# Performance work log

Hardware: AMD Instinct MI355X
Metric: run time of the kernel (lower is better)

Reference implementation:

```python
import jax, jax.numpy as jnp
import numpy as np
import itertools


def _dwconv(x, w, b, pad, dil):
    # depthwise conv3d, x: [B,C,H,W,D], w: [C,1,k,k,k]
    out = jax.lax.conv_general_dilated(
        x, w, (1, 1, 1), [(pad, pad)] * 3, rhs_dilation=(dil, dil, dil),
        dimension_numbers=('NCDHW', 'OIDHW', 'NCDHW'), feature_group_count=x.shape[1])
    return out + b[None, :, None, None, None]


def _conv(x, w, b, pad):
    out = jax.lax.conv_general_dilated(
        x, w, (1, 1, 1), [(pad, pad)] * 3,
        dimension_numbers=('NCDHW', 'OIDHW', 'NCDHW'))
    return out + b[None, :, None, None, None]


def _pw(x, w, b):
    # 1x1x1 conv: x [B,C,H,W,D], w [O,C]
    return jnp.einsum('bchwd,oc->bohwd', x, w) + b[None, :, None, None, None]


def _deform_conv3d(x, off_w, off_b, w, b):
    # DeformConvPack-style: offsets from a regular 3x3x3 conv, then
    # trilinearly-interpolated gather at (base + kernel tap + offset), then GEMM.
    B, C, H, W, D = x.shape
    K = 27
    dt = x.dtype
    off = _conv(x, off_w, off_b, 1).reshape(B, K, 3, H, W, D)  # per-tap (dh,dw,dd)
    gh = jnp.arange(H, dtype=dt)
    gw = jnp.arange(W, dtype=dt)
    gd = jnp.arange(D, dtype=dt)
    base = jnp.stack(jnp.meshgrid(gh, gw, gd, indexing='ij'), 0)  # [3,H,W,D]
    t = jnp.arange(-1, 2, dtype=dt)  # kernel taps, padding=1
    taps = jnp.stack(jnp.meshgrid(t, t, t, indexing='ij'), -1).reshape(K, 3)
    pos = base[None] + taps[:, :, None, None, None]  # [K,3,H,W,D]
    pos = pos[None] + off  # [B,K,3,H,W,D]
    i0 = jnp.floor(pos)
    frac = pos - i0  # [B,K,3,H,W,D]
    i0 = i0.astype(jnp.int32)
    N = H * W * D
    xf = x.reshape(B, C, N)
    hi = jnp.array([H - 1, W - 1, D - 1], jnp.int32)[None, None, :, None, None, None]
    acc = jnp.zeros((B, C, K * N), dt)
    for corner in itertools.product((0, 1), repeat=3):
        c = jnp.array(corner, jnp.int32)[None, None, :, None, None, None]
        idx = i0 + c
        wgt = jnp.prod(jnp.where(c == 1, frac, 1.0 - frac), axis=2)  # [B,K,H,W,D]
        valid = jnp.all((idx >= 0) & (idx <= hi), axis=2)
        ic = jnp.clip(idx, 0, hi)
        flat = (ic[:, :, 0] * W + ic[:, :, 1]) * D + ic[:, :, 2]  # [B,K,H,W,D]
        g = jnp.take_along_axis(xf, flat.reshape(B, 1, K * N), axis=2)  # [B,C,K*N]
        acc = acc + g * (wgt * valid.astype(dt)).reshape(B, 1, K * N)
    sampled = acc.reshape(B, C, K, N)
    out = jnp.einsum('bckn,ock->bon', sampled, w.reshape(w.shape[0], C, K))
    out = out + b[None, :, None]
    return out.reshape(B, -1, H, W, D)


def _forward(x, proj1_w, proj1_b, conv0_w, conv0_b, convsp_w, convsp_b,
             off_w, off_b, dcn_w, dcn_b, conv1_w, conv1_b, proj2_w, proj2_b,
             B, C, H, W, D):
    xv = jnp.transpose(x, (0, 2, 1)).reshape(B, C, H, W, D)
    shortcut = xv
    h = jax.nn.gelu(_pw(xv, proj1_w, proj1_b), approximate=False)
    u = h
    a = _dwconv(h, conv0_w, conv0_b, 2, 1)        # 5x5x5 depthwise
    a = _dwconv(a, convsp_w, convsp_b, 9, 3)      # 7x7x7 depthwise, dilation 3
    a = _deform_conv3d(a, off_w, off_b, dcn_w, dcn_b)
    a = _pw(a, conv1_w, conv1_b)
    h = u * a
    h = _pw(h, proj2_w, proj2_b)
    out = h + shortcut
    return jnp.transpose(out.reshape(B, C, H * W * D), (0, 2, 1))


def setup_inputs() -> dict:
    key = jax.random.key(0)
    ks = jax.random.split(key, 8)
    B, C, H, W, D = 1, 64, 32, 32, 32
    N = H * W * D
    r = lambda k, s, sc: jax.random.normal(k, s, jnp.float32) * np.float32(sc)
    inv = lambda f: 1.0 / np.sqrt(f)
    return {
        'x': jax.random.normal(ks[0], (B, N, C), jnp.float32),
        'proj1_w': r(ks[1], (C, C), inv(C)), 'proj1_b': jnp.zeros((C,), jnp.float32),
        'conv0_w': r(ks[2], (C, 1, 5, 5, 5), inv(125)), 'conv0_b': jnp.zeros((C,), jnp.float32),
        'convsp_w': r(ks[3], (C, 1, 7, 7, 7), inv(343)), 'convsp_b': jnp.zeros((C,), jnp.float32),
        'off_w': r(ks[4], (81, C, 3, 3, 3), 0.01 * inv(27 * C)), 'off_b': jnp.zeros((81,), jnp.float32),
        'dcn_w': r(ks[5], (C, C, 3, 3, 3), inv(27 * C)), 'dcn_b': jnp.zeros((C,), jnp.float32),
        'conv1_w': r(ks[6], (C, C), inv(C)), 'conv1_b': jnp.zeros((C,), jnp.float32),
        'proj2_w': r(ks[7], (C, C), inv(C)), 'proj2_b': jnp.zeros((C,), jnp.float32),
        'B': B, 'C': C, 'H': H, 'W': W, 'D': D,
    }


def reference(x, proj1_w, proj1_b, conv0_w, conv0_b, convsp_w, convsp_b,
              off_w, off_b, dcn_w, dcn_b, conv1_w, conv1_b, proj2_w, proj2_b,
              B, C, H, W, D):
    return _forward(x, proj1_w, proj1_b, conv0_w, conv0_b, convsp_w, convsp_b,
                    off_w, off_b, dcn_w, dcn_b, conv1_w, conv1_b, proj2_w, proj2_b,
                    B, C, H, W, D)
```

## Files before the change

### kernel.cpp

```cpp
#include <hip/hip_runtime.h>
#include <math.h>

#define NSP 32768
#define NCH 64

typedef _Float16 half8 __attribute__((ext_vector_type(8)));
typedef _Float16 half4 __attribute__((ext_vector_type(4)));
typedef _Float16 half2v __attribute__((ext_vector_type(2)));
typedef float f32x4 __attribute__((ext_vector_type(4)));

__global__ __launch_bounds__(256) void k_proj1m(const float* __restrict__ x,
        const half8* __restrict__ Wp1, const float* __restrict__ b,
        float* __restrict__ U) {
    __shared__ __align__(16) _Float16 Sx[64 * 72];
    int t = threadIdx.x;
    int n0 = blockIdx.x * 64;
    int lane = t & 63, wv = t >> 6;
    for (int i = wv; i < 64; i += 4) {
        float v = x[(size_t)(n0 + i) * 64 + lane];
        Sx[i * 72 + lane] = (_Float16)v;
    }
    __syncthreads();
    int pl = lane & 15, g = lane >> 4;
    int ob = wv;
    const half8* wbase = Wp1 + ob * 64 + lane;
    #pragma unroll
    for (int nt = 0; nt < 4; ++nt) {
        f32x4 acc4 = {0.f, 0.f, 0.f, 0.f};
        const _Float16* sb = &Sx[(nt * 16 + pl) * 72 + g * 8];
        #pragma unroll
        for (int kb = 0; kb < 2; ++kb) {
            half8 af = wbase[kb * 256];
            half8 bf = *(const half8*)(sb + kb * 32);
            acc4 = __builtin_amdgcn_mfma_f32_16x16x32_f16(af, bf, acc4, 0, 0, 0);
        }
        int n = n0 + nt * 16 + pl;
        #pragma unroll
        for (int r = 0; r < 4; ++r) {
            int o = ob * 16 + g * 4 + r;
            float a = acc4[r] + b[o];
            float gv = 0.5f * a * (1.0f + erff(a * 0.70710678118654752f));
            U[(size_t)o * NSP + n] = gv;
        }
    }
}

__global__ __launch_bounds__(256) void k_dw5(const float* __restrict__ in,
        const float* __restrict__ w, const float* __restrict__ b,
        float* __restrict__ out) {
    __shared__ float Sb5[2][20 * 38];
    int t = threadIdx.x;
    int bid = blockIdx.x;
    int blk = (bid & 7) * 128 + (bid >> 3);
    int c  = blk >> 4;
    int hq = (blk >> 1) & 7;
    int wq = blk & 1;
    int d  = t & 31;
    int wbloc = t >> 5;
    int wb = wq * 8 + wbloc;
    const float* wc = w + c * 125;
    const float* src = in + (size_t)c * NSP;

    for (int idx = t; idx < 160; idx += 256) {
        int bi = idx / 80, r = idx % 80;
        int wi = r >> 2, e = r & 3;
        int Dp = (e < 2) ? e : 32 + e;
        Sb5[bi][wi * 38 + Dp] = 0.f;
    }

    float bc = b[c];
    float acc[4][2];
    #pragma unroll
    for (int a = 0; a < 4; ++a) { acc[a][0] = bc; acc[a][1] = bc; }

    #define STAGE5(m)                                                        \
        { int hh_ = 4 * hq + (m) - 2;                                        \
          if ((unsigned)hh_ < 32u) {                                         \
            const float* row_ = src + (hh_ << 10);                           \
            for (int idx = t; idx < 160; idx += 256) {                       \
                int wi = idx >> 3, q = idx & 7;                              \
                int wj = 16 * wq - 2 + wi;                                   \
                float4 vv = make_float4(0.f, 0.f, 0.f, 0.f);                 \
                if ((unsigned)wj < 32u)                                      \
                    vv = *(const float4*)&row_[(wj << 5) + q * 4];           \
                float* dst = &Sb5[(m) & 1][wi * 38 + 2 + q * 4];             \
                dst[0] = vv.x; dst[1] = vv.y; dst[2] = vv.z; dst[3] = vv.w;  \
            } } }

    STAGE5(0)
    __syncthreads();
    #pragma unroll 1
    for (int m = 0; m < 8; ++m) {
        if (m < 7) STAGE5(m + 1)
        int hh = 4 * hq + m - 2;
        if ((unsigned)hh < 32u) {
            float v[6][5];
            const float* sb = &Sb5[m & 1][0];
            #pragma unroll
            for (int jc = 0; jc < 6; ++jc)
                #pragma unroll
                for (int l = 0; l < 5; ++l)
                    v[jc][l] = sb[(2 * wbloc + jc) * 38 + d + l];
            #pragma unroll
            for (int a = 0; a < 4; ++a) {
                if (a <= m && m <= a + 4) {
                    const float* wr = wc + (m - a) * 25;
                    float s0 = 0.f, s1 = 0.f;
                    #pragma unroll
                    for (int j = 0; j < 5; ++j)
                        #pragma unroll
                        for (int l = 0; l < 5; ++l) {
                            float wv2 = wr[j * 5 + l];
                            s0 += wv2 * v[j][l];
                            s1 += wv2 * v[j + 1][l];
                        }
                    acc[a][0] += s0;
                    acc[a][1] += s1;
                }
            }
        }
        __syncthreads();
    }
    #pragma unroll
    for (int a = 0; a < 4; ++a)
        #pragma unroll
        for (int bb = 0; bb < 2; ++bb)
            out[(size_t)c * NSP + ((4 * hq + a) << 10) + ((2 * wb + bb) << 5) + d]
                = acc[a][bb];
    #undef STAGE5
}

__global__ __launch_bounds__(256) void k_dw7(const float* __restrict__ in,
        const float* __restrict__ w, const float* __restrict__ b,
        float* __restrict__ out) {
    __shared__ float Sb7[2][26 * 52];
    int t = threadIdx.x;
    int bid = blockIdx.x;
    int blk = (bid & 7) * 96 + (bid >> 3);
    int c  = blk / 12;
    int h0 = (blk % 12) >> 2;
    int wq = blk & 3;
    int d  = t & 31;
    int wloc = t >> 5;
    int w_ = wq * 8 + wloc;
    const float* wc = w + c * 343;
    const float* src = in + (size_t)c * NSP;

    for (int idx = t; idx < 936; idx += 256) {
        int bi = idx / 468, r = idx % 468;
        int wi = r / 18, e = r % 18;
        int Dp = (e < 9) ? e : 32 + e;
        Sb7[bi][wi * 52 + Dp] = 0.f;
    }

    float bc = b[c];
    float acc[11];
    #pragma unroll
    for (int a = 0; a < 11; ++a) acc[a] = bc;

    #define STAGE7(m)                                                        \
        { int hh_ = h0 + 3 * (m) - 9;                                        \
          if ((unsigned)hh_ < 32u) {                                         \
            const float* row_ = src + (hh_ << 10);                           \
            for (int idx = t; idx < 208; idx += 256) {                       \
                int wi = idx >> 3, q = idx & 7;                              \
                int wj = 8 * wq - 9 + wi;                                    \
                float4 vv = make_float4(0.f, 0.f, 0.f, 0.f);                 \
                if ((unsigned)wj < 32u)                                      \
                    vv = *(const float4*)&row_[(wj << 5) + q * 4];           \
                float* dst = &Sb7[(m) & 1][wi * 52 + 9 + q * 4];             \
                dst[0] = vv.x; dst[1] = vv.y; dst[2] = vv.z; dst[3] = vv.w;  \
            } } }

    STAGE7(0)
    __syncthreads();
    #pragma unroll 1
    for (int m = 0; m < 17; ++m) {
        if (m < 16) STAGE7(m + 1)
        int hh = h0 + 3 * m - 9;
        if ((unsigned)hh < 32u) {
            float vf[49];
            const float* sb = &Sb7[m & 1][0];
            #pragma unroll
            for (int jw = 0; jw < 7; ++jw)
                #pragma unroll
                for (int l = 0; l < 7; ++l)
                    vf[jw * 7 + l] = sb[(wloc + 3 * jw) * 52 + d + 3 * l];
            #pragma unroll
            for (int a = 0; a < 11; ++a) {
                if (a <= m && m <= a + 6) {
                    const float* wr = wc + (m - a) * 49;
                    float sA = 0.f, sB = 0.f;
                    #pragma unroll
                    for (int q = 0; q < 24; ++q) {
                        sA = fmaf(wr[2 * q],     vf[2 * q],     sA);
                        sB = fmaf(wr[2 * q + 1], vf[2 * q + 1], sB);
                    }
                    acc[a] += sA + sB + wr[48] * vf[48];
                }
            }
        }
        __syncthreads();
    }
    #pragma unroll
    for (int a = 0; a < 11; ++a) {
        int h = h0 + 3 * a;
        if (h < 32)
            out[(size_t)c * NSP + (h << 10) + (w_ << 5) + d] = acc[a];
    }
    #undef STAGE7
}

__global__ __launch_bounds__(256) void k_tr(const float* __restrict__ in,
        _Float16* __restrict__ outh) {
    __shared__ float tile[64 * 65];
    int t = threadIdx.x;
    int n0 = blockIdx.x * 64;
    for (int i = 0; i < 16; ++i) {
        int idx = i * 256 + t;
        int c = idx >> 6, nl = idx & 63;
        tile[c * 65 + nl] = in[(size_t)c * NSP + n0 + nl];
    }
    __syncthreads();
    for (int i = 0; i < 16; ++i) {
        int idx = i * 256 + t;
        int nl = idx >> 6, c = idx & 63;
        outh[(size_t)(n0 + nl) * 64 + c] = (_Float16)tile[c * 65 + nl];
    }
}

__global__ __launch_bounds__(256) void k_wpack(const float* __restrict__ dw,
        _Float16* __restrict__ Wp) {
    int idx = blockIdx.x * 256 + threadIdx.x;
    int j = idx & 7;
    int l = (idx >> 3) & 63;
    int obk = idx >> 9;
    int ob = obk & 3, kb = obk >> 2;
    int o = ob * 16 + (l & 15);
    int Kp = kb * 32 + (l >> 4) * 8 + j;
    int k = Kp >> 6, c = Kp & 63;
    Wp[idx] = (_Float16)dw[(size_t)o * 1728 + c * 27 + k];
}

__global__ __launch_bounds__(256) void k_wpack_off(const float* __restrict__ ow,
        _Float16* __restrict__ Wp2) {
    int idx = blockIdx.x * 256 + threadIdx.x;
    int j = idx & 7;
    int l = (idx >> 3) & 63;
    int obk = idx >> 9;
    int ob = obk % 6, kb = obk / 6;
    int o = ob * 16 + (l & 15);
    int Kp = kb * 32 + (l >> 4) * 8 + j;
    int k = Kp >> 6, c = Kp & 63;
    Wp2[idx] = (o < 81) ? (_Float16)ow[(size_t)o * 1728 + c * 27 + k]
                        : (_Float16)0.f;
}

__global__ __launch_bounds__(256) void k_wpack64(const float* __restrict__ w,
        _Float16* __restrict__ Wp) {
    int idx = blockIdx.x * 256 + threadIdx.x;
    int j = idx & 7;
    int l = (idx >> 3) & 63;
    int obk = idx >> 9;
    int ob = obk & 3, kb = obk >> 2;
    int o = ob * 16 + (l & 15);
    int Kp = kb * 32 + (l >> 4) * 8 + j;
    Wp[idx] = (_Float16)w[o * 64 + Kp];
}

__global__ __launch_bounds__(384) void k_offg(const _Float16* __restrict__ aTh,
        const half8* __restrict__ Wp2, const float* __restrict__ obias,
        float* __restrict__ off) {
    __shared__ __align__(16) _Float16 S2[2][4 * 34 * 72];
    int t = threadIdx.x;
    int bid = blockIdx.x;
    int blk = (bid & 7) * 64 + (bid >> 3);
    int h = blk >> 4, w0 = (blk & 15) * 2;
    int n0 = (h << 10) + (w0 << 5);
    int lane = t & 63, wv = t >> 6;
    int co8 = (lane & 7) << 3;

    for (int u = t; u < 1152; u += 384) {
        int bi = u / 576, r2 = u % 576;
        int nbw = r2 / 144, r3 = r2 % 144;
        int dd = (r3 >= 72) ? 33 : 0, cc = r3 % 72;
        S2[bi][(nbw * 34 + dd) * 72 + cc] = (_Float16)0.f;
    }

    int pl = lane & 15, g = lane >> 4;
    int obi = wv;
    f32x4 acc[4];
    #pragma unroll
    for (int i = 0; i < 4; ++i) acc[i] = (f32x4){0.f, 0.f, 0.f, 0.f};
    const half8* wb = Wp2 + obi * 64 + lane;

    #define OSTAGE(kh)                                                        \
        { int hh_ = h + (kh) - 1;                                            \
          bool okh_ = (unsigned)hh_ < 32u;                                   \
          for (int u = wv; u < 16; u += 6) {                                 \
              int nbw = u >> 2, oct = u & 3;                                 \
              int wj = w0 + nbw - 1;                                         \
              int di = oct * 8 + (lane >> 3);                                \
              bool ok = okh_ & ((unsigned)wj < 32u);                         \
              half8 vv = (half8)(_Float16)0.f;                               \
              if (ok) vv = *(const half8*)(aTh +                             \
                  ((size_t)((((hh_ << 5) + wj) << 5) + di)) * 64 + co8);     \
              *(half8*)&S2[(kh) & 1][(nbw * 34 + 1 + di) * 72 + co8] = vv;   \
          } }

    #define OCOMP(kh)                                                        \
        { const _Float16* sb = &S2[(kh) & 1][pl * 72 + g * 8];               \
          _Pragma("unroll")                                                  \
          for (int kk = 0; kk < 18; ++kk) {                                  \
              int kglob = (kh) * 9 + (kk >> 1);                              \
              int kw3 = (kglob / 3) % 3, kd = kglob % 3;                     \
              half8 af = wb[(size_t)((kh) * 18 + kk) * 384];                 \
              _Pragma("unroll")                                              \
              for (int pt = 0; pt < 4; ++pt) {                               \
                  int row = ((pt >> 1) + kw3) * 34 + (pt & 1) * 16 + kd;     \
                  half8 bf = *(const half8*)(sb + row * 72 + (kk & 1) * 32); \
                  acc[pt] = __builtin_amdgcn_mfma_f32_16x16x32_f16(          \
                                af, bf, acc[pt], 0, 0, 0);                   \
              }                                                              \
          } }

    OSTAGE(0)
    __syncthreads();
    OSTAGE(1)
    OCOMP(0)
    __syncthreads();
    OSTAGE(2)
    OCOMP(1)
    __syncthreads();
    OCOMP(2)
    #undef OSTAGE
    #undef OCOMP

    #pragma unroll
    for (int pt = 0; pt < 4; ++pt) {
        #pragma unroll
        for (int r = 0; r < 4; ++r) {
            int o = obi * 16 + g * 4 + r;
            if (o < 81)
                off[(size_t)o * NSP + n0 + pt * 16 + pl] = acc[pt][r] + obias[o];
        }
    }
}

__global__ __launch_bounds__(256) void k_deform(const _Float16* __restrict__ aTh,
        const float* __restrict__ off, const half8* __restrict__ Wp,
        const float* __restrict__ db, float* __restrict__ dcn) {
    __shared__ __align__(16) _Float16 S[32 * 456];
    __shared__ __align__(16) _Float16 TPF[864 * 4];
    __shared__ int TPv[864];
    int t = threadIdx.x;
    int bid = blockIdx.x;
    int blk = (bid & 7) * 128 + (bid >> 3);
    int n0 = blk * 32;
    int lane = t & 63, wv = t >> 6;

    for (int idx = t; idx < 864; idx += 256) {
        int p = idx & 31, k = idx >> 5;
        int n = n0 + p;
        int h = n >> 10, w = (n >> 5) & 31, d = n & 31;
        float ph = (float)(h + k / 9 - 1)       + off[(size_t)(k * 3 + 0) * NSP + n];
        float pw = (float)(w + (k / 3) % 3 - 1) + off[(size_t)(k * 3 + 1) * NSP + n];
        float pd = (float)(d + k % 3 - 1)       + off[(size_t)(k * 3 + 2) * NSP + n];
        float fh = floorf(ph), fw = floorf(pw), fd = floorf(pd);
        int ih = (int)fh, iw = (int)fw, id = (int)fd;
        int nb0 = ih * 1024 + iw * 32 + id;
        int mask = 0;
        #pragma unroll
        for (int cb = 0; cb < 8; ++cb) {
            int hh = ih + ((cb >> 2) & 1);
            int wq = iw + ((cb >> 1) & 1);
            int dq = id + (cb & 1);
            bool ok = ((unsigned)hh < 32u) & ((unsigned)wq < 32u) & ((unsigned)dq < 32u);
            mask |= (ok ? 1 : 0) << cb;
        }
        TPv[idx] = ((nb0 + 4096) << 8) | mask;
        half4 f;
        f[0] = (_Float16)(ph - fh);
        f[1] = (_Float16)(pw - fw);
        f[2] = (_Float16)(pd - fd);
        f[3] = (_Float16)0.f;
        *(half4*)&TPF[idx * 4] = f;
    }
    __syncthreads();

    int p8 = lane >> 3, co = lane & 7;
    int pl = lane & 15, g = lane >> 4;
    f32x4 acc[2];
    acc[0] = (f32x4){0.f, 0.f, 0.f, 0.f};
    acc[1] = (f32x4){0.f, 0.f, 0.f, 0.f};
    const half8* wbase = Wp + wv * 64 + lane;
    const _Float16* sbase0 = &S[pl * 456 + g * 8];
    const _Float16* sbase1 = &S[(16 + pl) * 456 + g * 8];

    #define DCHUNK(T0, NT)                                                   \
        for (int u = wv; u < (NT) * 4; u += 4) {                             \
            int kk = u >> 2, pg = u & 3;                                     \
            int p = pg * 8 + p8;                                             \
            int tap = ((T0) + kk) * 32 + p;                                  \
            int v = TPv[tap];                                                \
            int nb = (v >> 8) - 4096, mask = v & 255;                        \
            half4 f = *(const half4*)&TPF[tap * 4];                          \
            _Float16 one = (_Float16)1.f;                                    \
            _Float16 rh = f[0], rw = f[1], rd = f[2];                        \
            _Float16 h0 = one - rh, w0 = one - rw, d0 = one - rd;            \
            _Float16 t00 = h0 * w0, t01 = h0 * rw;                           \
            _Float16 t10 = rh * w0, t11 = rh * rw;                           \
            half2v a0 = (half2v)0, a1 = (half2v)0, a2 = (half2v)0,           \
                   a3 = (half2v)0;                                           \
            _Pragma("unroll")                                                \
            for (int i = 0; i < 8; ++i) {                                    \
                int nn = nb + ((i >> 2) & 1) * 1024 + ((i >> 1) & 1) * 32    \
                       + (i & 1);                                            \
                bool okc = (mask >> i) & 1;                                  \
                size_t ad = okc ? ((size_t)nn << 6) : 0;                     \
                half8 vv = *(const half8*)(aTh + ad + (co << 3));            \
                _Float16 txy = (i & 4) ? ((i & 2) ? t11 : t10)               \
                                       : ((i & 2) ? t01 : t00);              \
                _Float16 wg = txy * ((i & 1) ? rd : d0);                     \
                wg = okc ? wg : (_Float16)0.f;                               \
                half2v wg2 = {wg, wg};                                       \
                a0 += (half2v){vv[0], vv[1]} * wg2;                          \
                a1 += (half2v){vv[2], vv[3]} * wg2;                          \
                a2 += (half2v){vv[4], vv[5]} * wg2;                          \
                a3 += (half2v){vv[6], vv[7]} * wg2;                          \
            }                                                                \
            half8 r;                                                         \
            r[0] = a0[0]; r[1] = a0[1]; r[2] = a1[0]; r[3] = a1[1];          \
            r[4] = a2[0]; r[5] = a2[1]; r[6] = a3[0]; r[7] = a3[1];          \
            *(half8*)&S[p * 456 + kk * 64 + (co << 3)] = r;                  \
        }                                                                    \
        __syncthreads();                                                     \
        _Pragma("unroll")                                                    \
        for (int kb = 0; kb < (NT) * 2; ++kb) {                              \
            half8 af = wbase[(size_t)(2 * (T0) + kb) * 256];                 \
            half8 bf0 = *(const half8*)(sbase0 + kb * 32);                   \
            half8 bf1 = *(const half8*)(sbase1 + kb * 32);                   \
            acc[0] = __builtin_amdgcn_mfma_f32_16x16x32_f16(af, bf0,         \
                         acc[0], 0, 0, 0);                                   \
            acc[1] = __builtin_amdgcn_mfma_f32_16x16x32_f16(af, bf1,         \
                         acc[1], 0, 0, 0);                                   \
        }                                                                    \
        __syncthreads();

    DCHUNK(0, 7)
    DCHUNK(7, 7)
    DCHUNK(14, 7)
    DCHUNK(21, 6)
    #undef DCHUNK

    #pragma unroll
    for (int pt = 0; pt < 2; ++pt) {
        #pragma unroll
        for (int r2 = 0; r2 < 4; ++r2) {
            int o = wv * 16 + g * 4 + r2;
            dcn[(size_t)o * NSP + n0 + pt * 16 + pl] = acc[pt][r2] + db[o];
        }
    }
}

__global__ __launch_bounds__(256) void k_finalm(const float* __restrict__ dcn,
        const float* __restrict__ U, const float* __restrict__ x,
        const half8* __restrict__ Wc1, const float* __restrict__ c1b,
        const half8* __restrict__ Wp2f, const float* __restrict__ p2b,
        float* __restrict__ out) {
    __shared__ __align__(16) _Float16 Sd[64 * 72];
    __shared__ __align__(16) _Float16 Sh[64 * 72];
    int t = threadIdx.x;
    int n0 = blockIdx.x * 64;
    int lane = t & 63, wv = t >> 6;
    for (int i = wv; i < 64; i += 4) {
        float v = dcn[(size_t)i * NSP + n0 + lane];
        Sd[lane * 72 + i] = (_Float16)v;
    }
    __syncthreads();

    int pl = lane & 15, g = lane >> 4;
    int ob = wv;
    const half8* w1 = Wc1 + ob * 64 + lane;
    #pragma unroll
    for (int nt = 0; nt < 4; ++nt) {
        f32x4 acc4 = {0.f, 0.f, 0.f, 0.f};
        const _Float16* sb = &Sd[(nt * 16 + pl) * 72 + g * 8];
        #pragma unroll
        for (int kb = 0; kb < 2; ++kb) {
            half8 af = w1[kb * 256];
            half8 bf = *(const half8*)(sb + kb * 32);
            acc4 = __builtin_amdgcn_mfma_f32_16x16x32_f16(af, bf, acc4, 0, 0, 0);
        }
        int n = n0 + nt * 16 + pl;
        int o0 = ob * 16 + g * 4;
        float4 bb = *(const float4*)&c1b[o0];
        half4 hv;
        hv[0] = (_Float16)(U[(size_t)(o0 + 0) * NSP + n] * (acc4[0] + bb.x));
        hv[1] = (_Float16)(U[(size_t)(o0 + 1) * NSP + n] * (acc4[1] + bb.y));
        hv[2] = (_Float16)(U[(size_t)(o0 + 2) * NSP + n] * (acc4[2] + bb.z));
        hv[3] = (_Float16)(U[(size_t)(o0 + 3) * NSP + n] * (acc4[3] + bb.w));
        *(half4*)&Sh[(nt * 16 + pl) * 72 + o0] = hv;
    }
    __syncthreads();

    const half8* w2 = Wp2f + ob * 64 + lane;
    #pragma unroll
    for (int nt = 0; nt < 4; ++nt) {
        f32x4 acc4 = {0.f, 0.f, 0.f, 0.f};
        const _Float16* sb = &Sh[(nt * 16 + pl) * 72 + g * 8];
        #pragma unroll
        for (int kb = 0; kb < 2; ++kb) {
            half8 af = w2[kb * 256];
            half8 bf = *(const half8*)(sb + kb * 32);
            acc4 = __builtin_amdgcn_mfma_f32_16x16x32_f16(af, bf, acc4, 0, 0, 0);
        }
        int n = n0 + nt * 16 + pl;
        int o0 = ob * 16 + g * 4;
        float4 bb = *(const float4*)&p2b[o0];
        float4 xr = *(const float4*)&x[(size_t)n * 64 + o0];
        float4 ov;
        ov.x = acc4[0] + bb.x + xr.x;
        ov.y = acc4[1] + bb.y + xr.y;
        ov.z = acc4[2] + bb.z + xr.z;
        ov.w = acc4[3] + bb.w + xr.w;
        *(float4*)&out[(size_t)n * 64 + o0] = ov;
    }
}

extern "C" void kernel_launch(void* const* d_in, const int* in_sizes, int n_in,
                              void* d_out, int out_size, void* d_ws, size_t ws_size,
                              hipStream_t stream) {
    const float* x   = (const float*)d_in[0];
    const float* p1w = (const float*)d_in[1];
    const float* p1b = (const float*)d_in[2];
    const float* c0w = (const float*)d_in[3];
    const float* c0b = (const float*)d_in[4];
    const float* csw = (const float*)d_in[5];
    const float* csb = (const float*)d_in[6];
    const float* ofw = (const float*)d_in[7];
    const float* ofb = (const float*)d_in[8];
    const float* dcw = (const float*)d_in[9];
    const float* dcb = (const float*)d_in[10];
    const float* c1w = (const float*)d_in[11];
    const float* c1b = (const float*)d_in[12];
    const float* p2w = (const float*)d_in[13];
    const float* p2b = (const float*)d_in[14];
    float* out = (float*)d_out;

    char* ws = (char*)d_ws;
    const size_t CN4 = (size_t)NCH * NSP * 4;
    float* U    = (float*)(ws);
    float* T0   = (float*)(ws + CN4);
    float* T1   = (float*)(ws + 2 * CN4);
    float* OFFp = (float*)(ws + 4 * CN4);
    float* DCN  = (float*)(ws + 4 * CN4 + (size_t)81 * NSP * 4);
    _Float16* Wp   = (_Float16*)(ws + 5 * CN4 + (size_t)81 * NSP * 4);
    _Float16* Wp2  = Wp + 110592;
    _Float16* Wp1  = Wp2 + 165888;
    _Float16* Wc1  = Wp1 + 4096;
    _Float16* Wp2f = Wc1 + 4096;
    _Float16* aTh  = (_Float16*)T0;

    k_wpack64  <<<16, 256, 0, stream>>>(p1w, Wp1);
    k_wpack64  <<<16, 256, 0, stream>>>(c1w, Wc1);
    k_wpack64  <<<16, 256, 0, stream>>>(p2w, Wp2f);
    k_wpack    <<<432, 256, 0, stream>>>(dcw, Wp);
    k_wpack_off<<<648, 256, 0, stream>>>(ofw, Wp2);
    k_proj1m   <<<NSP / 64, 256, 0, stream>>>(x, (const half8*)Wp1, p1b, U);
    k_dw5      <<<1024, 256, 0, stream>>>(U, c0w, c0b, T0);
    k_dw7      <<<768, 256, 0, stream>>>(T0, csw, csb, T1);
    k_tr       <<<NSP / 64, 256, 0, stream>>>(T1, aTh);
    k_offg     <<<512, 384, 0, stream>>>(aTh, (const half8*)Wp2, ofb, OFFp);
    k_deform   <<<1024, 256, 0, stream>>>(aTh, OFFp, (const half8*)Wp, dcb, DCN);
    k_finalm   <<<NSP / 64, 256, 0, stream>>>(DCN, U, x, (const half8*)Wc1, c1b,
                                              (const half8*)Wp2f, p2b, out);
}
```

Before: 131.3 us.

## Store intermediate activations in fp16 and emit deform output point-major

Intermediate buffers (GELU output U, the depthwise conv outputs, and the deform-conv output) are now stored as fp16 instead of fp32, halving their global memory traffic. The depthwise kernels load half8 vectors and widen them to fp32 in shared memory. The transpose kernel now moves fp16 data in 16-byte vectors. The deform kernel writes its output point-major so the final kernel can load it with vector reads instead of a strided transpose. The cost is extra rounding on intermediates that were previously kept in fp32.

```diff
diff --git a/kernel.cpp b/kernel.cpp
--- a/kernel.cpp
+++ b/kernel.cpp
@@ -11,7 +11,7 @@
 
 __global__ __launch_bounds__(256) void k_proj1m(const float* __restrict__ x,
         const half8* __restrict__ Wp1, const float* __restrict__ b,
-        float* __restrict__ U) {
+        _Float16* __restrict__ Uh) {
     __shared__ __align__(16) _Float16 Sx[64 * 72];
     int t = threadIdx.x;
     int n0 = blockIdx.x * 64;
@@ -40,14 +40,14 @@
             int o = ob * 16 + g * 4 + r;
             float a = acc4[r] + b[o];
             float gv = 0.5f * a * (1.0f + erff(a * 0.70710678118654752f));
-            U[(size_t)o * NSP + n] = gv;
-        }
-    }
-}
-
-__global__ __launch_bounds__(256) void k_dw5(const float* __restrict__ in,
+            Uh[(size_t)o * NSP + n] = (_Float16)gv;
+        }
+    }
+}
+
+__global__ __launch_bounds__(256) void k_dw5(const _Float16* __restrict__ in,
         const float* __restrict__ w, const float* __restrict__ b,
-        float* __restrict__ out) {
+        _Float16* __restrict__ out) {
     __shared__ float Sb5[2][20 * 38];
     int t = threadIdx.x;
     int bid = blockIdx.x;
@@ -59,7 +59,7 @@
     int wbloc = t >> 5;
     int wb = wq * 8 + wbloc;
     const float* wc = w + c * 125;
-    const float* src = in + (size_t)c * NSP;
+    const _Float16* src = in + ((size_t)c << 15);
 
     for (int idx = t; idx < 160; idx += 256) {
         int bi = idx / 80, r = idx % 80;
@@ -76,15 +76,18 @@
     #define STAGE5(m)                                                        \
         { int hh_ = 4 * hq + (m) - 2;                                        \
           if ((unsigned)hh_ < 32u) {                                         \
-            const float* row_ = src + (hh_ << 10);                           \
-            for (int idx = t; idx < 160; idx += 256) {                       \
-                int wi = idx >> 3, q = idx & 7;                              \
+            const _Float16* row_ = src + (hh_ << 10);                        \
+            for (int idx = t; idx < 80; idx += 256) {                        \
+                int wi = idx >> 2, oct = idx & 3;                            \
                 int wj = 16 * wq - 2 + wi;                                   \
-                float4 vv = make_float4(0.f, 0.f, 0.f, 0.f);                 \
+                half8 vv = (half8)(_Float16)0.f;                             \
                 if ((unsigned)wj < 32u)                                      \
-                    vv = *(const float4*)&row_[(wj << 5) + q * 4];           \
-                float* dst = &Sb5[(m) & 1][wi * 38 + 2 + q * 4];             \
-                dst[0] = vv.x; dst[1] = vv.y; dst[2] = vv.z; dst[3] = vv.w;  \
+                    vv = *(const half8*)&row_[(wj << 5) + oct * 8];          \
+                float* dst = &Sb5[(m) & 1][wi * 38 + 2 + oct * 8];           \
+                dst[0] = (float)vv[0]; dst[1] = (float)vv[1];                \
+                dst[2] = (float)vv[2]; dst[3] = (float)vv[3];                \
+                dst[4] = (float)vv[4]; dst[5] = (float)vv[5];                \
+                dst[6] = (float)vv[6]; dst[7] = (float)vv[7];                \
             } } }
 
     STAGE5(0)
@@ -126,13 +129,13 @@
         #pragma unroll
         for (int bb = 0; bb < 2; ++bb)
             out[(size_t)c * NSP + ((4 * hq + a) << 10) + ((2 * wb + bb) << 5) + d]
-                = acc[a][bb];
+                = (_Float16)acc[a][bb];
     #undef STAGE5
 }
 
-__global__ __launch_bounds__(256) void k_dw7(const float* __restrict__ in,
+__global__ __launch_bounds__(256) void k_dw7(const _Float16* __restrict__ in,
         const float* __restrict__ w, const float* __restrict__ b,
-        float* __restrict__ out) {
+        _Float16* __restrict__ out) {
     __shared__ float Sb7[2][26 * 52];
     int t = threadIdx.x;
     int bid = blockIdx.x;
@@ -144,7 +147,7 @@
     int wloc = t >> 5;
     int w_ = wq * 8 + wloc;
     const float* wc = w + c * 343;
-    const float* src = in + (size_t)c * NSP;
+    const _Float16* src = in + ((size_t)c << 15);
 
     for (int idx = t; idx < 936; idx += 256) {
         int bi = idx / 468, r = idx % 468;
@@ -161,15 +164,18 @@
     #define STAGE7(m)                                                        \
         { int hh_ = h0 + 3 * (m) - 9;                                        \
           if ((unsigned)hh_ < 32u) {                                         \
-            const float* row_ = src + (hh_ << 10);                           \
-            for (int idx = t; idx < 208; idx += 256) {                       \
-                int wi = idx >> 3, q = idx & 7;                              \
+            const _Float16* row_ = src + (hh_ << 10);                        \
+            for (int idx = t; idx < 104; idx += 256) {                       \
+                int wi = idx >> 2, oct = idx & 3;                            \
                 int wj = 8 * wq - 9 + wi;                                    \
-                float4 vv = make_float4(0.f, 0.f, 0.f, 0.f);                 \
+                half8 vv = (half8)(_Float16)0.f;                             \
                 if ((unsigned)wj < 32u)                                      \
-                    vv = *(const float4*)&row_[(wj << 5) + q * 4];           \
-                float* dst = &Sb7[(m) & 1][wi * 52 + 9 + q * 4];             \
-                dst[0] = vv.x; dst[1] = vv.y; dst[2] = vv.z; dst[3] = vv.w;  \
+                    vv = *(const half8*)&row_[(wj << 5) + oct * 8];          \
+                float* dst = &Sb7[(m) & 1][wi * 52 + 9 + oct * 8];           \
+                dst[0] = (float)vv[0]; dst[1] = (float)vv[1];                \
+                dst[2] = (float)vv[2]; dst[3] = (float)vv[3];                \
+                dst[4] = (float)vv[4]; dst[5] = (float)vv[5];                \
+                dst[6] = (float)vv[6]; dst[7] = (float)vv[7];                \
             } } }
 
     STAGE7(0)
@@ -206,26 +212,32 @@
     for (int a = 0; a < 11; ++a) {
         int h = h0 + 3 * a;
         if (h < 32)
-            out[(size_t)c * NSP + (h << 10) + (w_ << 5) + d] = acc[a];
+            out[(size_t)c * NSP + (h << 10) + (w_ << 5) + d] = (_Float16)acc[a];
     }
     #undef STAGE7
 }
 
-__global__ __launch_bounds__(256) void k_tr(const float* __restrict__ in,
+__global__ __launch_bounds__(256) void k_tr(const _Float16* __restrict__ in,
         _Float16* __restrict__ outh) {
-    __shared__ float tile[64 * 65];
+    __shared__ __align__(16) _Float16 tile[64 * 74];
     int t = threadIdx.x;
     int n0 = blockIdx.x * 64;
-    for (int i = 0; i < 16; ++i) {
-        int idx = i * 256 + t;
-        int c = idx >> 6, nl = idx & 63;
-        tile[c * 65 + nl] = in[(size_t)c * NSP + n0 + nl];
-    }
-    __syncthreads();
-    for (int i = 0; i < 16; ++i) {
-        int idx = i * 256 + t;
-        int nl = idx >> 6, c = idx & 63;
-        outh[(size_t)(n0 + nl) * 64 + c] = (_Float16)tile[c * 65 + nl];
+    #pragma unroll
+    for (int i = 0; i < 2; ++i) {
+        int u = i * 256 + t;
+        int c = u >> 3, oct = u & 7;
+        half8 v = *(const half8*)&in[(size_t)c * NSP + n0 + oct * 8];
+        *(half8*)&tile[c * 74 + oct * 8] = v;
+    }
+    __syncthreads();
+    #pragma unroll
+    for (int i = 0; i < 2; ++i) {
+        int u = i * 256 + t;
+        int nl = u >> 3, co = u & 7;
+        half8 r;
+        #pragma unroll
+        for (int j = 0; j < 8; ++j) r[j] = tile[(co * 8 + j) * 74 + nl];
+        *(half8*)&outh[(size_t)(n0 + nl) * 64 + co * 8] = r;
     }
 }
 
@@ -349,7 +361,7 @@
 
 __global__ __launch_bounds__(256) void k_deform(const _Float16* __restrict__ aTh,
         const float* __restrict__ off, const half8* __restrict__ Wp,
-        const float* __restrict__ db, float* __restrict__ dcn) {
+        const float* __restrict__ db, _Float16* __restrict__ dcnT) {
     __shared__ __align__(16) _Float16 S[32 * 456];
     __shared__ __align__(16) _Float16 TPF[864 * 4];
     __shared__ int TPv[864];
@@ -455,16 +467,18 @@
 
     #pragma unroll
     for (int pt = 0; pt < 2; ++pt) {
+        half4 hv;
         #pragma unroll
         for (int r2 = 0; r2 < 4; ++r2) {
             int o = wv * 16 + g * 4 + r2;
-            dcn[(size_t)o * NSP + n0 + pt * 16 + pl] = acc[pt][r2] + db[o];
-        }
-    }
-}
-
-__global__ __launch_bounds__(256) void k_finalm(const float* __restrict__ dcn,
-        const float* __restrict__ U, const float* __restrict__ x,
+            hv[r2] = (_Float16)(acc[pt][r2] + db[o]);
+        }
+        *(half4*)&dcnT[(size_t)(n0 + pt * 16 + pl) * 64 + wv * 16 + g * 4] = hv;
+    }
+}
+
+__global__ __launch_bounds__(256) void k_finalm(const _Float16* __restrict__ dcnT,
+        const _Float16* __restrict__ Uh, const float* __restrict__ x,
         const half8* __restrict__ Wc1, const float* __restrict__ c1b,
         const half8* __restrict__ Wp2f, const float* __restrict__ p2b,
         float* __restrict__ out) {
@@ -473,9 +487,12 @@
     int t = threadIdx.x;
     int n0 = blockIdx.x * 64;
     int lane = t & 63, wv = t >> 6;
-    for (int i = wv; i < 64; i += 4) {
-        float v = dcn[(size_t)i * NSP + n0 + lane];
-        Sd[lane * 72 + i] = (_Float16)v;
+    #pragma unroll
+    for (int i = 0; i < 2; ++i) {
+        int u = i * 256 + t;
+        int nl = u >> 3, oct = u & 7;
+        *(half8*)&Sd[nl * 72 + oct * 8] =
+            *(const half8*)&dcnT[(size_t)(n0 + nl) * 64 + oct * 8];
     }
     __syncthreads();
 
@@ -496,10 +513,10 @@
         int o0 = ob * 16 + g * 4;
         float4 bb = *(const float4*)&c1b[o0];
         half4 hv;
-        hv[0] = (_Float16)(U[(size_t)(o0 + 0) * NSP + n] * (acc4[0] + bb.x));
-        hv[1] = (_Float16)(U[(size_t)(o0 + 1) * NSP + n] * (acc4[1] + bb.y));
-        hv[2] = (_Float16)(U[(size_t)(o0 + 2) * NSP + n] * (acc4[2] + bb.z));
-        hv[3] = (_Float16)(U[(size_t)(o0 + 3) * NSP + n] * (acc4[3] + bb.w));
+        hv[0] = (_Float16)((float)Uh[(size_t)(o0 + 0) * NSP + n] * (acc4[0] + bb.x));
+        hv[1] = (_Float16)((float)Uh[(size_t)(o0 + 1) * NSP + n] * (acc4[1] + bb.y));
+        hv[2] = (_Float16)((float)Uh[(size_t)(o0 + 2) * NSP + n] * (acc4[2] + bb.z));
+        hv[3] = (_Float16)((float)Uh[(size_t)(o0 + 3) * NSP + n] * (acc4[3] + bb.w));
         *(half4*)&Sh[(nt * 16 + pl) * 72 + o0] = hv;
     }
     __syncthreads();
@@ -549,30 +566,30 @@
     float* out = (float*)d_out;
 
     char* ws = (char*)d_ws;
-    const size_t CN4 = (size_t)NCH * NSP * 4;
-    float* U    = (float*)(ws);
-    float* T0   = (float*)(ws + CN4);
-    float* T1   = (float*)(ws + 2 * CN4);
-    float* OFFp = (float*)(ws + 4 * CN4);
-    float* DCN  = (float*)(ws + 4 * CN4 + (size_t)81 * NSP * 4);
-    _Float16* Wp   = (_Float16*)(ws + 5 * CN4 + (size_t)81 * NSP * 4);
+    const size_t CN2 = (size_t)NCH * NSP * 2;
+    _Float16* Uh   = (_Float16*)(ws);
+    _Float16* T0h  = (_Float16*)(ws + CN2);
+    _Float16* T1h  = (_Float16*)(ws + 2 * CN2);
+    _Float16* aTh  = (_Float16*)(ws + 3 * CN2);
+    float*    OFFp = (float*)(ws + 4 * CN2);
+    _Float16* dcnT = (_Float16*)(ws + 4 * CN2 + (size_t)81 * NSP * 4);
+    _Float16* Wp   = dcnT + (size_t)NSP * 64;
     _Float16* Wp2  = Wp + 110592;
     _Float16* Wp1  = Wp2 + 165888;
     _Float16* Wc1  = Wp1 + 4096;
     _Float16* Wp2f = Wc1 + 4096;
-    _Float16* aTh  = (_Float16*)T0;
 
     k_wpack64  <<<16, 256, 0, stream>>>(p1w, Wp1);
     k_wpack64  <<<16, 256, 0, stream>>>(c1w, Wc1);
     k_wpack64  <<<16, 256, 0, stream>>>(p2w, Wp2f);
     k_wpack    <<<432, 256, 0, stream>>>(dcw, Wp);
     k_wpack_off<<<648, 256, 0, stream>>>(ofw, Wp2);
-    k_proj1m   <<<NSP / 64, 256, 0, stream>>>(x, (const half8*)Wp1, p1b, U);
-    k_dw5      <<<1024, 256, 0, stream>>>(U, c0w, c0b, T0);
-    k_dw7      <<<768, 256, 0, stream>>>(T0, csw, csb, T1);
-    k_tr       <<<NSP / 64, 256, 0, stream>>>(T1, aTh);
+    k_proj1m   <<<NSP / 64, 256, 0, stream>>>(x, (const half8*)Wp1, p1b, Uh);
+    k_dw5      <<<1024, 256, 0, stream>>>(Uh, c0w, c0b, T0h);
+    k_dw7      <<<768, 256, 0, stream>>>(T0h, csw, csb, T1h);
+    k_tr       <<<NSP / 64, 256, 0, stream>>>(T1h, aTh);
     k_offg     <<<512, 384, 0, stream>>>(aTh, (const half8*)Wp2, ofb, OFFp);
-    k_deform   <<<1024, 256, 0, stream>>>(aTh, OFFp, (const half8*)Wp, dcb, DCN);
-    k_finalm   <<<NSP / 64, 256, 0, stream>>>(DCN, U, x, (const half8*)Wc1, c1b,
+    k_deform   <<<1024, 256, 0, stream>>>(aTh, OFFp, (const half8*)Wp, dcb, dcnT);
+    k_finalm   <<<NSP / 64, 256, 0, stream>>>(dcnT, Uh, x, (const half8*)Wc1, c1b,
                                               (const half8*)Wp2f, p2b, out);
 }
```

Measured after the change: 125.5 us. 4.5% less time.
